# Optimization experiments

Hardware: AMD Instinct MI355X
Metric: run time of the kernel (lower is better)

## Reference

```python
import math
import jax, jax.numpy as jnp
import numpy as np

HIDDEN = 2048
NUM_HEADS = 16
HEAD_DIM = HIDDEN // NUM_HEADS  # 128
KV_RANK = 512
ROPE_DIM = 64
MAX_POS = 131072
ORIG_POS = 8192
BASE = 500000.0
BETA_FAST, BETA_SLOW = 32.0, 1.0
B, S = 2, 2048
EPS = 1e-6


def yarn_inv_freq():
    scaling = MAX_POS / ORIG_POS
    pos_freqs = BASE ** (np.arange(0, ROPE_DIM, 2, dtype=np.float64) / ROPE_DIM)
    extrap = 1.0 / pos_freqs
    interp = 1.0 / (scaling * pos_freqs)
    low = max(math.floor(ROPE_DIM * math.log(ORIG_POS / (BETA_FAST * 2 * math.pi)) / (2 * math.log(BASE))), 0)
    high = min(math.ceil(ROPE_DIM * math.log(ORIG_POS / (BETA_SLOW * 2 * math.pi)) / (2 * math.log(BASE))), ROPE_DIM - 1)
    i = np.arange(ROPE_DIM // 2, dtype=np.float64)
    smooth = np.clip((i - low) / max(high - low, 1), 0.0, 1.0)
    inv_freq = (1.0 - smooth) * interp + smooth * extrap
    return np.asarray(inv_freq, dtype=np.float32)


def yarn_cos_sin(seq_len, dtype):
    inv_freq = jnp.asarray(yarn_inv_freq())  # [rope/2]
    pos = jnp.arange(seq_len, dtype=jnp.float32)
    freqs = pos[:, None] * inv_freq[None, :]          # [S, rope/2]
    emb = jnp.concatenate([freqs, freqs], axis=-1)    # [S, rope]
    scaling = MAX_POS / ORIG_POS
    mscale = (0.1 * math.log(scaling) + 1.0) if scaling > 1 else 1.0
    cos = (jnp.cos(emb) * mscale).astype(dtype)[None]  # [1, S, rope]
    sin = (jnp.sin(emb) * mscale).astype(dtype)[None]
    return cos, sin


def rotate_half(x):
    x1, x2 = jnp.split(x, 2, axis=-1)
    return jnp.concatenate([-x2, x1], axis=-1)


def rms_norm(x, w):
    xf = x.astype(jnp.float32)
    var = jnp.mean(xf * xf, axis=-1, keepdims=True)
    return (w * (xf * jax.lax.rsqrt(var + EPS))).astype(x.dtype)


def setup_inputs() -> dict:
    key = jax.random.key(0)
    ks = jax.random.split(key, 5)
    return {
        'hidden_states': jax.random.normal(ks[0], (B, S, HIDDEN), jnp.float32),
        'q_w': jax.random.normal(ks[1], (NUM_HEADS * HEAD_DIM, HIDDEN), jnp.float32) * 0.02,
        'kv_a_w': jax.random.normal(ks[2], (KV_RANK + ROPE_DIM, HIDDEN), jnp.float32) * 0.02,
        'kv_b_w': jax.random.normal(ks[3], (NUM_HEADS * HEAD_DIM * 2, KV_RANK), jnp.float32) * 0.02,
        'o_w': jax.random.normal(ks[4], (HIDDEN, NUM_HEADS * HEAD_DIM), jnp.float32) * 0.02,
        'kv_norm_w': jnp.ones((KV_RANK,), jnp.float32),
    }


def reference(hidden_states, q_w, kv_a_w, kv_b_w, o_w, kv_norm_w):
    b, s, _ = hidden_states.shape
    # Q projection -> [B, H, S, D]
    q = hidden_states @ q_w.T
    q = q.reshape(b, s, NUM_HEADS, HEAD_DIM).transpose(0, 2, 1, 3)
    # KV compression: split off rope part (unused, matching source) and latent
    kv_compress = hidden_states @ kv_a_w.T               # [B, S, rope + rank]
    kv_latent = kv_compress[..., ROPE_DIM:]              # [B, S, rank]
    kv_latent = rms_norm(kv_latent, kv_norm_w)
    kv = kv_latent @ kv_b_w.T                            # [B, S, H*D*2]
    kv = kv.reshape(b, s, NUM_HEADS, 2, HEAD_DIM)
    k = kv[:, :, :, 0].transpose(0, 2, 1, 3)             # [B, H, S, D]
    v = kv[:, :, :, 1].transpose(0, 2, 1, 3)
    # Partial RoPE on first ROPE_DIM dims
    cos, sin = yarn_cos_sin(s, q.dtype)                  # [1, S, rope]
    cos = cos[:, None]                                   # [1, 1, S, rope]
    sin = sin[:, None]
    q_pe, k_pe = q[..., :ROPE_DIM], k[..., :ROPE_DIM]
    q_pe = q_pe * cos + rotate_half(q_pe) * sin
    k_pe = k_pe * cos + rotate_half(k_pe) * sin
    q = jnp.concatenate([q_pe, q[..., ROPE_DIM:]], axis=-1)
    k = jnp.concatenate([k_pe, k[..., ROPE_DIM:]], axis=-1)
    # SDPA (no mask), softmax in fp32
    scale = HEAD_DIM ** -0.5
    scores = jnp.einsum('bhqd,bhkd->bhqk', q, k) * scale
    attn = jax.nn.softmax(scores.astype(jnp.float32), axis=-1).astype(q.dtype)
    out = jnp.einsum('bhqk,bhkd->bhqd', attn, v)         # [B, H, S, D]
    out = out.transpose(0, 2, 1, 3).reshape(b, s, NUM_HEADS * HEAD_DIM)
    return out @ o_w.T
```

## Files before the change

### kernel.cpp

```cpp
#include <hip/hip_runtime.h>

typedef unsigned short u16;
typedef unsigned int u32;
typedef __attribute__((ext_vector_type(4))) float f32x4;
typedef __attribute__((ext_vector_type(8))) short short8;

#define S_LEN 2048
#define BATCH 2
#define HID 2048
#define NH 16
#define HD 128
#define KVR 512
#define TOKENS 4096
#define QSCALE 0.12751879523243842f

__device__ __forceinline__ u32 f2bf(float f) {
  u32 b = __float_as_uint(f);
  return (b + 0x7FFFu + ((b >> 16) & 1u)) >> 16;
}
__device__ __forceinline__ float bf2f(u16 u) {
  return __uint_as_float(((u32)u) << 16);
}
__device__ __forceinline__ void gl16(const void* g, void* l) {
  __builtin_amdgcn_global_load_lds((const __attribute__((address_space(1))) void*)g,
                                   (__attribute__((address_space(3))) void*)l, 16, 0, 0);
}
__device__ __forceinline__ u32 cvtpk(float a, float b) {
  u32 r;
  asm("v_cvt_pk_bf16_f32 %0, %1, %2" : "=v"(r) : "v"(a), "v"(b));
  return r;
}

__global__ __launch_bounds__(256) void convert_f32_bf16(const float* __restrict__ in,
                                                        u16* __restrict__ out, int n4) {
  int stride = gridDim.x * blockDim.x;
  for (int i = blockIdx.x * blockDim.x + threadIdx.x; i < n4; i += stride) {
    float4 v = reinterpret_cast<const float4*>(in)[i];
    uint2 o;
    o.x = f2bf(v.x) | (f2bf(v.y) << 16);
    o.y = f2bf(v.z) | (f2bf(v.w) << 16);
    reinterpret_cast<uint2*>(out)[i] = o;
  }
}

__global__ __launch_bounds__(256) void yarn_table(float2* __restrict__ cs) {
  int idx = blockIdx.x * blockDim.x + threadIdx.x;
  if (idx >= S_LEN * 32) return;
  int pos = idx >> 5, i = idx & 31;
  double pf = pow(500000.0, (double)i / 32.0);
  double sm = ((double)i - 9.0) / 9.0;
  sm = sm < 0.0 ? 0.0 : (sm > 1.0 ? 1.0 : sm);
  double invf = (1.0 - sm) / (16.0 * pf) + sm / pf;
  float f = (float)pos * (float)invf;
  const float mscale = 1.2772588722239781f;
  cs[idx] = make_float2(cosf(f) * mscale, sinf(f) * mscale);
}

__global__ __launch_bounds__(256) void rmsnorm_kernel(const float* __restrict__ X,
                                                      const float* __restrict__ w,
                                                      u16* __restrict__ out) {
  int wid = threadIdx.x >> 6, lane = threadIdx.x & 63;
  int row = blockIdx.x * 4 + wid;
  const float* xr = X + (size_t)row * KVR;
  float4 v0 = reinterpret_cast<const float4*>(xr)[lane * 2];
  float4 v1 = reinterpret_cast<const float4*>(xr)[lane * 2 + 1];
  float ss = v0.x * v0.x + v0.y * v0.y + v0.z * v0.z + v0.w * v0.w +
             v1.x * v1.x + v1.y * v1.y + v1.z * v1.z + v1.w * v1.w;
  #pragma unroll
  for (int m = 1; m < 64; m <<= 1) ss += __shfl_xor(ss, m);
  float sc = rsqrtf(ss * (1.0f / KVR) + 1e-6f);
  const float* wr = w + lane * 8;
  uint4 o;
  o.x = f2bf(v0.x * sc * wr[0]) | (f2bf(v0.y * sc * wr[1]) << 16);
  o.y = f2bf(v0.z * sc * wr[2]) | (f2bf(v0.w * sc * wr[3]) << 16);
  o.z = f2bf(v1.x * sc * wr[4]) | (f2bf(v1.y * sc * wr[5]) << 16);
  o.w = f2bf(v1.z * sc * wr[6]) | (f2bf(v1.w * sc * wr[7]) << 16);
  reinterpret_cast<uint4*>(out)[(size_t)row * 64 + lane] = o;
}

__global__ __launch_bounds__(256) void vtrans_kernel(const u16* __restrict__ kv,
                                                     u16* __restrict__ Vt) {
  __shared__ u16 T[128 * 128];
  const int bh = blockIdx.y, b = bh >> 4, h = bh & 15;
  const int s0 = blockIdx.x * 128;
  const int tid = threadIdx.x;
  const u16* src = kv + ((size_t)(b * S_LEN + s0)) * 4096 + h * 256 + 128;
  #pragma unroll
  for (int c = 0; c < 8; ++c) {
    int u = c * 256 + tid;
    int row = u >> 4, slot = u & 15;
    uint4 v = *reinterpret_cast<const uint4*>(src + (size_t)row * 4096 + slot * 8);
    *reinterpret_cast<uint4*>(&T[row * 128 + ((slot ^ (row & 7)) << 3)]) = v;
  }
  __syncthreads();
  #pragma unroll
  for (int c = 0; c < 8; ++c) {
    int u = c * 256 + tid;
    int d = u >> 4, j = u & 15;
    u16 tmp[8] __attribute__((aligned(16)));
    #pragma unroll
    for (int i = 0; i < 8; ++i) {
      int s = j * 8 + i;
      tmp[i] = T[s * 128 + (((d >> 3) ^ (s & 7)) << 3) + (d & 7)];
    }
    *reinterpret_cast<uint4*>(Vt + ((size_t)bh * 128 + d) * S_LEN + s0 + j * 8) =
        *reinterpret_cast<const uint4*>(tmp);
  }
}

template<int MODE>
__global__ __launch_bounds__(256) void gemm_bt(const u16* __restrict__ A,
                                               const u16* __restrict__ W,
                                               void* __restrict__ C0v,
                                               void* __restrict__ C1v,
                                               const float2* __restrict__ cs,
                                               int M, int N, int K) {
  __shared__ u16 As[128 * 32];
  __shared__ u16 Bs[128 * 32];
  const int tid = threadIdx.x;
  const int wid = tid >> 6;
  const int lane = tid & 63;
  const int r16 = lane & 15;
  const int kg = lane >> 4;
  const int bm = blockIdx.y * 128;
  const int bn = blockIdx.x * 128;
  const int wm = (wid >> 1) * 64;
  const int wn = (wid & 1) * 64;
  f32x4 acc[4][4] = {};
  const int srow = tid >> 2;
  const int sslot = tid & 3;
  const int ra = srow, rb = 64 + srow;
  const int ca = sslot ^ ((ra >> 1) & 3);
  const int cb = sslot ^ ((rb >> 1) & 3);
  const u16* a0 = A + (size_t)(bm + ra) * K + ca * 8;
  const u16* a1 = A + (size_t)(bm + rb) * K + cb * 8;
  const u16* b0 = W + (size_t)(bn + ra) * K + ca * 8;
  const u16* b1 = W + (size_t)(bn + rb) * K + cb * 8;

  for (int kt = 0; kt < K; kt += 32) {
    gl16(a0 + kt, &As[wid * 512]);
    gl16(a1 + kt, &As[wid * 512 + 2048]);
    gl16(b0 + kt, &Bs[wid * 512]);
    gl16(b1 + kt, &Bs[wid * 512 + 2048]);
    __syncthreads();
    short8 af[4], bfv[4];
    #pragma unroll
    for (int mi = 0; mi < 4; ++mi) {
      int row = wm + mi * 16 + r16;
      af[mi] = *reinterpret_cast<const short8*>(&As[row * 32 + ((kg ^ ((row >> 1) & 3)) << 3)]);
    }
    #pragma unroll
    for (int ni = 0; ni < 4; ++ni) {
      int row = wn + ni * 16 + r16;
      bfv[ni] = *reinterpret_cast<const short8*>(&Bs[row * 32 + ((kg ^ ((row >> 1) & 3)) << 3)]);
    }
    #pragma unroll
    for (int mi = 0; mi < 4; ++mi)
      #pragma unroll
      for (int ni = 0; ni < 4; ++ni)
        acc[mi][ni] = __builtin_amdgcn_mfma_f32_16x16x32_bf16(af[mi], bfv[ni], acc[mi][ni], 0, 0, 0);
    __syncthreads();
  }

  if (MODE == 2 || MODE == 3) {
    const bool doRope = (wn == 0) && (MODE == 2 ? (bn < 2048) : ((bn & 128) == 0));
    if (doRope) {
      #pragma unroll
      for (int mi = 0; mi < 4; ++mi) {
        const int t0 = bm + wm + mi * 16 + kg * 4;
        #pragma unroll
        for (int r = 0; r < 4; ++r) {
          const int pos = (t0 + r) & (S_LEN - 1);
          #pragma unroll
          for (int np = 0; np < 2; ++np) {
            float2 c = cs[pos * 32 + np * 16 + r16];
            float x1 = acc[mi][np][r], x2 = acc[mi][np + 2][r];
            acc[mi][np][r] = x1 * c.x - x2 * c.y;
            acc[mi][np + 2][r] = x2 * c.x + x1 * c.y;
          }
        }
      }
    }
  }

  if (MODE == 1) {
    float* C = (float*)C0v;
    #pragma unroll
    for (int mi = 0; mi < 4; ++mi)
      #pragma unroll
      for (int ni = 0; ni < 4; ++ni) {
        size_t base = (size_t)(bm + wm + mi * 16 + kg * 4) * N + (bn + wn + ni * 16 + r16);
        #pragma unroll
        for (int r = 0; r < 4; ++r) C[base + (size_t)r * N] = acc[mi][ni][r];
      }
  } else if (MODE == 2) {
    if (bn < 2048) {
      u16* C = (u16*)C0v;
      #pragma unroll
      for (int mi = 0; mi < 4; ++mi)
        #pragma unroll
        for (int ni = 0; ni < 4; ++ni) {
          size_t base = (size_t)(bm + wm + mi * 16 + kg * 4) * HID + (bn + wn + ni * 16 + r16);
          #pragma unroll
          for (int r = 0; r < 4; ++r) C[base + (size_t)r * HID] = (u16)f2bf(acc[mi][ni][r] * QSCALE);
        }
    } else {
      float* C = (float*)C1v;
      #pragma unroll
      for (int mi = 0; mi < 4; ++mi)
        #pragma unroll
        for (int ni = 0; ni < 4; ++ni) {
          size_t base = (size_t)(bm + wm + mi * 16 + kg * 4) * KVR +
                        (bn - 2048 + wn + ni * 16 + r16);
          #pragma unroll
          for (int r = 0; r < 4; ++r) C[base + (size_t)r * KVR] = acc[mi][ni][r];
        }
    }
  } else {
    u16* C = (u16*)C0v;
    #pragma unroll
    for (int mi = 0; mi < 4; ++mi)
      #pragma unroll
      for (int ni = 0; ni < 4; ++ni) {
        size_t base = (size_t)(bm + wm + mi * 16 + kg * 4) * N + (bn + wn + ni * 16 + r16);
        #pragma unroll
        for (int r = 0; r < 4; ++r) C[base + (size_t)r * N] = (u16)f2bf(acc[mi][ni][r]);
      }
  }
}

#define KVB 64
__global__ __launch_bounds__(256) void attn_kernel(const u16* __restrict__ Q,
                                                   const u16* __restrict__ KV,
                                                   const u16* __restrict__ Vt,
                                                   u16* __restrict__ O) {
  __shared__ u16 Ks[2][KVB * 128];
  __shared__ u16 Vs[2][128 * KVB];
  __shared__ u16 Ps[4][2][16 * 64];
  const int tid = threadIdx.x, wid = tid >> 6, lane = tid & 63;
  const int r16 = lane & 15, kg = lane >> 4;
  const int bh = blockIdx.x, b = bh >> 4, h = bh & 15;
  const int q0 = blockIdx.y * 128 + wid * 32;

  short8 qf0[4], qf1[4];
  {
    const size_t qr0 = ((size_t)(b * S_LEN) + q0 + r16) * HID + h * HD;
    #pragma unroll
    for (int ds = 0; ds < 4; ++ds) {
      qf0[ds] = *reinterpret_cast<const short8*>(&Q[qr0 + ds * 32 + kg * 8]);
      qf1[ds] = *reinterpret_cast<const short8*>(&Q[qr0 + (size_t)16 * HID + ds * 32 + kg * 8]);
    }
  }
  asm volatile("s_waitcnt vmcnt(0)" ::: "memory");

  f32x4 oacc0[8] = {}, oacc1[8] = {};
  float m0 = -3.0e38f, l0 = 0.0f, m1 = -3.0e38f, l1 = 0.0f;

  const int krow = wid * 4 + (lane >> 4);
  const int kslot = (lane & 15) ^ (krow & 7);
  const u16* gK = KV + (size_t)(b * S_LEN) * 4096 + h * 256 + (size_t)krow * 4096 + kslot * 8;
  const int vrow = wid * 8 + (lane >> 3);
  const int vslot = (lane & 7) ^ (vrow & 7);
  const u16* gV = Vt + ((size_t)bh * 128 + vrow) * S_LEN + vslot * 8;

  auto stage = [&](int buf, int it) {
    const int k0 = it * KVB;
    #pragma unroll
    for (int c = 0; c < 4; ++c) {
      gl16(gK + (size_t)(k0 + c * 16) * 4096, &Ks[buf][(c * 256 + wid * 64) * 8]);
      gl16(gV + (size_t)c * 32 * S_LEN + k0, &Vs[buf][(c * 256 + wid * 64) * 8]);
    }
  };

  auto qk = [&](const u16* Kc, short8 (&qf)[4], f32x4 (&sc)[4]) {
    #pragma unroll
    for (int nt = 0; nt < 4; ++nt) {
      sc[nt] = (f32x4){0.f, 0.f, 0.f, 0.f};
      const int key = nt * 16 + r16;
      #pragma unroll
      for (int ds = 0; ds < 4; ++ds) {
        short8 kf = *reinterpret_cast<const short8*>(
            &Kc[key * 128 + (((ds * 4 + kg) ^ (r16 & 7)) << 3)]);
        sc[nt] = __builtin_amdgcn_mfma_f32_16x16x32_bf16(kf, qf[ds], sc[nt], 0, 0, 0);
      }
    }
  };

  auto softmax_store = [&](f32x4 (&sc)[4], float& mreg, float& lreg, f32x4 (&oa)[8],
                           u16* psbase) {
    float mx = fmaxf(fmaxf(fmaxf(sc[0][0], sc[0][1]), fmaxf(sc[0][2], sc[0][3])),
                     fmaxf(fmaxf(sc[1][0], sc[1][1]), fmaxf(sc[1][2], sc[1][3])));
    mx = fmaxf(mx, fmaxf(fmaxf(fmaxf(sc[2][0], sc[2][1]), fmaxf(sc[2][2], sc[2][3])),
                         fmaxf(fmaxf(sc[3][0], sc[3][1]), fmaxf(sc[3][2], sc[3][3]))));
    mx = fmaxf(mx, __shfl_xor(mx, 16));
    mx = fmaxf(mx, __shfl_xor(mx, 32));
    if (!__all(mx - mreg <= 8.0f)) {
      float nm = fmaxf(mreg, mx);
      float al = __builtin_amdgcn_exp2f(mreg - nm);
      mreg = nm;
      lreg *= al;
      float ar0 = __shfl(al, kg * 4 + 0), ar1 = __shfl(al, kg * 4 + 1);
      float ar2 = __shfl(al, kg * 4 + 2), ar3 = __shfl(al, kg * 4 + 3);
      #pragma unroll
      for (int db = 0; db < 8; ++db) {
        oa[db][0] *= ar0; oa[db][1] *= ar1; oa[db][2] *= ar2; oa[db][3] *= ar3;
      }
    }
    const float nm = mreg;
    float s0 = 0.f;
    #pragma unroll
    for (int nt = 0; nt < 4; ++nt) {
      float p0 = __builtin_amdgcn_exp2f(sc[nt][0] - nm);
      float p1 = __builtin_amdgcn_exp2f(sc[nt][1] - nm);
      float p2 = __builtin_amdgcn_exp2f(sc[nt][2] - nm);
      float p3 = __builtin_amdgcn_exp2f(sc[nt][3] - nm);
      s0 += (p0 + p1) + (p2 + p3);
      uint2 pk;
      pk.x = cvtpk(p0, p1);
      pk.y = cvtpk(p2, p3);
      *reinterpret_cast<uint2*>(
          &psbase[(r16 * 64 + nt * 16 + kg * 4) ^ ((r16 & 7) << 3)]) = pk;
    }
    s0 += __shfl_xor(s0, 16);
    s0 += __shfl_xor(s0, 32);
    lreg += s0;
  };

  stage(0, 0);
  for (int it = 0; it < S_LEN / KVB; ++it) {
    const int cur = it & 1;
    if (it + 1 < S_LEN / KVB) {
      stage(cur ^ 1, it + 1);
      asm volatile("s_waitcnt vmcnt(8)" ::: "memory");
    } else {
      asm volatile("s_waitcnt vmcnt(0)" ::: "memory");
    }
    __builtin_amdgcn_s_barrier();

    const u16* Kc = &Ks[cur][0];
    f32x4 sc[4];
    qk(Kc, qf0, sc);
    softmax_store(sc, m0, l0, oacc0, &Ps[wid][0][0]);
    __builtin_amdgcn_sched_barrier(0);
    qk(Kc, qf1, sc);
    softmax_store(sc, m1, l1, oacc1, &Ps[wid][1][0]);
    __builtin_amdgcn_sched_barrier(0);

    const u16* Vc = &Vs[cur][0];
    #pragma unroll
    for (int ks = 0; ks < 2; ++ks) {
      const int pidx = (r16 * 64 + ks * 32 + kg * 8) ^ ((r16 & 7) << 3);
      short8 pa0 = *reinterpret_cast<const short8*>(&Ps[wid][0][pidx]);
      short8 pa1 = *reinterpret_cast<const short8*>(&Ps[wid][1][pidx]);
      #pragma unroll
      for (int db = 0; db < 8; ++db) {
        const int drow = db * 16 + r16;
        short8 vf = *reinterpret_cast<const short8*>(
            &Vc[drow * 64 + (((ks * 4 + kg) ^ (r16 & 7)) << 3)]);
        oacc0[db] = __builtin_amdgcn_mfma_f32_16x16x32_bf16(pa0, vf, oacc0[db], 0, 0, 0);
        oacc1[db] = __builtin_amdgcn_mfma_f32_16x16x32_bf16(pa1, vf, oacc1[db], 0, 0, 0);
      }
    }
    __builtin_amdgcn_s_barrier();
  }

  {
    float li0 = 1.0f / l0, li1 = 1.0f / l1;
    float lr0[4], lr1[4];
    #pragma unroll
    for (int r = 0; r < 4; ++r) {
      lr0[r] = __shfl(li0, kg * 4 + r);
      lr1[r] = __shfl(li1, kg * 4 + r);
    }
    #pragma unroll
    for (int db = 0; db < 8; ++db)
      #pragma unroll
      for (int r = 0; r < 4; ++r) {
        size_t i0 = ((size_t)(b * S_LEN) + q0 + kg * 4 + r) * HID + h * HD + db * 16 + r16;
        O[i0] = (u16)f2bf(oacc0[db][r] * lr0[r]);
        O[i0 + (size_t)16 * HID] = (u16)f2bf(oacc1[db][r] * lr1[r]);
      }
  }
}

extern "C" void kernel_launch(void* const* d_in, const int* in_sizes, int n_in,
                              void* d_out, int out_size, void* d_ws, size_t ws_size,
                              hipStream_t stream) {
  (void)in_sizes; (void)n_in; (void)out_size; (void)ws_size;
  const float* hidden = (const float*)d_in[0];
  const float* q_w    = (const float*)d_in[1];
  const float* kv_a_w = (const float*)d_in[2];
  const float* kv_b_w = (const float*)d_in[3];
  const float* o_w    = (const float*)d_in[4];
  const float* nw     = (const float*)d_in[5];

  char* ws = (char*)d_ws;
  size_t off = 0;
  auto carve = [&](size_t n) { void* p = ws + off; off += (n + 255) & ~(size_t)255; return p; };
  u16* h_bf    = (u16*)carve((size_t)TOKENS * HID * 2);
  u16* qaw_bf  = (u16*)carve((size_t)2560 * HID * 2);
  u16* kvbw_bf = (u16*)carve((size_t)4096 * KVR * 2);
  u16* ow_bf   = (u16*)carve((size_t)HID * HID * 2);
  u16* q_bf    = (u16*)carve((size_t)TOKENS * HID * 2);
  float* lat_f = (float*)carve((size_t)TOKENS * KVR * 4);
  u16* lat_bf  = (u16*)carve((size_t)TOKENS * KVR * 2);
  u16* kv_bf   = (u16*)carve((size_t)TOKENS * 4096 * 2);
  float2* cs_t = (float2*)carve((size_t)S_LEN * 32 * 8);
  u16* attn_bf = (u16*)carve((size_t)TOKENS * HID * 2);
  u16* vt_bf   = h_bf;

  dim3 blk(256);
  auto cg = [](int n4) { int g = (n4 + 255) / 256; return dim3(g > 2048 ? 2048 : g); };

  convert_f32_bf16<<<cg(TOKENS * HID / 4), blk, 0, stream>>>(hidden, h_bf, TOKENS * HID / 4);
  convert_f32_bf16<<<cg(HID * HID / 4), blk, 0, stream>>>(q_w, qaw_bf, HID * HID / 4);
  convert_f32_bf16<<<cg(KVR * HID / 4), blk, 0, stream>>>(kv_a_w + 64 * HID,
                                                          qaw_bf + (size_t)2048 * HID,
                                                          KVR * HID / 4);
  convert_f32_bf16<<<cg(4096 * KVR / 4), blk, 0, stream>>>(kv_b_w, kvbw_bf, 4096 * KVR / 4);
  convert_f32_bf16<<<cg(HID * HID / 4), blk, 0, stream>>>(o_w, ow_bf, HID * HID / 4);
  yarn_table<<<dim3(S_LEN * 32 / 256), blk, 0, stream>>>(cs_t);

  gemm_bt<2><<<dim3(2560 / 128, TOKENS / 128), blk, 0, stream>>>(
      h_bf, qaw_bf, q_bf, lat_f, cs_t, TOKENS, 2560, HID);
  rmsnorm_kernel<<<dim3(TOKENS / 4), blk, 0, stream>>>(lat_f, nw, lat_bf);
  gemm_bt<3><<<dim3(4096 / 128, TOKENS / 128), blk, 0, stream>>>(
      lat_bf, kvbw_bf, kv_bf, nullptr, cs_t, TOKENS, 4096, KVR);

  vtrans_kernel<<<dim3(S_LEN / 128, BATCH * NH), blk, 0, stream>>>(kv_bf, vt_bf);

  attn_kernel<<<dim3(BATCH * NH, S_LEN / 128), blk, 0, stream>>>(q_bf, kv_bf, vt_bf, attn_bf);

  gemm_bt<1><<<dim3(HID / 128, TOKENS / 128), blk, 0, stream>>>(
      attn_bf, ow_bf, (float*)d_out, nullptr, cs_t, TOKENS, HID, HID);
}
```

Baseline: 304.9 us.

## Use 32x32 MFMA in attention and fuse V transpose into kv GEMM epilogue

```diff
diff --git a/kernel.cpp b/kernel.cpp
--- a/kernel.cpp
+++ b/kernel.cpp
@@ -3,6 +3,7 @@
 typedef unsigned short u16;
 typedef unsigned int u32;
 typedef __attribute__((ext_vector_type(4))) float f32x4;
+typedef __attribute__((ext_vector_type(16))) float f32x16;
 typedef __attribute__((ext_vector_type(8))) short short8;
 
 #define S_LEN 2048
@@ -76,36 +77,6 @@
   o.z = f2bf(v1.x * sc * wr[4]) | (f2bf(v1.y * sc * wr[5]) << 16);
   o.w = f2bf(v1.z * sc * wr[6]) | (f2bf(v1.w * sc * wr[7]) << 16);
   reinterpret_cast<uint4*>(out)[(size_t)row * 64 + lane] = o;
-}
-
-__global__ __launch_bounds__(256) void vtrans_kernel(const u16* __restrict__ kv,
-                                                     u16* __restrict__ Vt) {
-  __shared__ u16 T[128 * 128];
-  const int bh = blockIdx.y, b = bh >> 4, h = bh & 15;
-  const int s0 = blockIdx.x * 128;
-  const int tid = threadIdx.x;
-  const u16* src = kv + ((size_t)(b * S_LEN + s0)) * 4096 + h * 256 + 128;
-  #pragma unroll
-  for (int c = 0; c < 8; ++c) {
-    int u = c * 256 + tid;
-    int row = u >> 4, slot = u & 15;
-    uint4 v = *reinterpret_cast<const uint4*>(src + (size_t)row * 4096 + slot * 8);
-    *reinterpret_cast<uint4*>(&T[row * 128 + ((slot ^ (row & 7)) << 3)]) = v;
-  }
-  __syncthreads();
-  #pragma unroll
-  for (int c = 0; c < 8; ++c) {
-    int u = c * 256 + tid;
-    int d = u >> 4, j = u & 15;
-    u16 tmp[8] __attribute__((aligned(16)));
-    #pragma unroll
-    for (int i = 0; i < 8; ++i) {
-      int s = j * 8 + i;
-      tmp[i] = T[s * 128 + (((d >> 3) ^ (s & 7)) << 3) + (d & 7)];
-    }
-    *reinterpret_cast<uint4*>(Vt + ((size_t)bh * 128 + d) * S_LEN + s0 + j * 8) =
-        *reinterpret_cast<const uint4*>(tmp);
-  }
 }
 
 template<int MODE>
@@ -216,6 +187,35 @@
           for (int r = 0; r < 4; ++r) C[base + (size_t)r * KVR] = acc[mi][ni][r];
         }
     }
+  } else if (MODE == 3) {
+    if ((bn & 128) == 0) {
+      u16* C = (u16*)C0v;
+      #pragma unroll
+      for (int mi = 0; mi < 4; ++mi)
+        #pragma unroll
+        for (int ni = 0; ni < 4; ++ni) {
+          size_t base = (size_t)(bm + wm + mi * 16 + kg * 4) * N + (bn + wn + ni * 16 + r16);
+          #pragma unroll
+          for (int r = 0; r < 4; ++r) C[base + (size_t)r * N] = (u16)f2bf(acc[mi][ni][r]);
+        }
+    } else {
+      u16* Vt = (u16*)C1v;
+      const int hh = bn >> 8;
+      #pragma unroll
+      for (int mi = 0; mi < 4; ++mi) {
+        const int tok0 = bm + wm + mi * 16 + kg * 4;
+        const int bb = tok0 >> 11, s = tok0 & (S_LEN - 1);
+        #pragma unroll
+        for (int ni = 0; ni < 4; ++ni) {
+          const int d = wn + ni * 16 + r16;
+          uint2 pk;
+          pk.x = cvtpk(acc[mi][ni][0], acc[mi][ni][1]);
+          pk.y = cvtpk(acc[mi][ni][2], acc[mi][ni][3]);
+          *reinterpret_cast<uint2*>(
+              &Vt[((size_t)((bb * 16 + hh) * 128 + d)) * S_LEN + s]) = pk;
+        }
+      }
+    }
   } else {
     u16* C = (u16*)C0v;
     #pragma unroll
@@ -236,25 +236,23 @@
                                                    u16* __restrict__ O) {
   __shared__ u16 Ks[2][KVB * 128];
   __shared__ u16 Vs[2][128 * KVB];
-  __shared__ u16 Ps[4][2][16 * 64];
+  __shared__ u16 Ps[4][32 * 64];
   const int tid = threadIdx.x, wid = tid >> 6, lane = tid & 63;
-  const int r16 = lane & 15, kg = lane >> 4;
+  const int q = lane & 31, hi = lane >> 5;
   const int bh = blockIdx.x, b = bh >> 4, h = bh & 15;
   const int q0 = blockIdx.y * 128 + wid * 32;
 
-  short8 qf0[4], qf1[4];
+  short8 qf[8];
   {
-    const size_t qr0 = ((size_t)(b * S_LEN) + q0 + r16) * HID + h * HD;
-    #pragma unroll
-    for (int ds = 0; ds < 4; ++ds) {
-      qf0[ds] = *reinterpret_cast<const short8*>(&Q[qr0 + ds * 32 + kg * 8]);
-      qf1[ds] = *reinterpret_cast<const short8*>(&Q[qr0 + (size_t)16 * HID + ds * 32 + kg * 8]);
-    }
+    const size_t qr = ((size_t)(b * S_LEN) + q0 + q) * HID + h * HD;
+    #pragma unroll
+    for (int ds = 0; ds < 8; ++ds)
+      qf[ds] = *reinterpret_cast<const short8*>(&Q[qr + ds * 16 + hi * 8]);
   }
   asm volatile("s_waitcnt vmcnt(0)" ::: "memory");
 
-  f32x4 oacc0[8] = {}, oacc1[8] = {};
-  float m0 = -3.0e38f, l0 = 0.0f, m1 = -3.0e38f, l1 = 0.0f;
+  f32x16 oacc[4] = {};
+  float m = -3.0e38f, l = 0.0f;
 
   const int krow = wid * 4 + (lane >> 4);
   const int kslot = (lane & 15) ^ (krow & 7);
@@ -270,60 +268,6 @@
       gl16(gK + (size_t)(k0 + c * 16) * 4096, &Ks[buf][(c * 256 + wid * 64) * 8]);
       gl16(gV + (size_t)c * 32 * S_LEN + k0, &Vs[buf][(c * 256 + wid * 64) * 8]);
     }
-  };
-
-  auto qk = [&](const u16* Kc, short8 (&qf)[4], f32x4 (&sc)[4]) {
-    #pragma unroll
-    for (int nt = 0; nt < 4; ++nt) {
-      sc[nt] = (f32x4){0.f, 0.f, 0.f, 0.f};
-      const int key = nt * 16 + r16;
-      #pragma unroll
-      for (int ds = 0; ds < 4; ++ds) {
-        short8 kf = *reinterpret_cast<const short8*>(
-            &Kc[key * 128 + (((ds * 4 + kg) ^ (r16 & 7)) << 3)]);
-        sc[nt] = __builtin_amdgcn_mfma_f32_16x16x32_bf16(kf, qf[ds], sc[nt], 0, 0, 0);
-      }
-    }
-  };
-
-  auto softmax_store = [&](f32x4 (&sc)[4], float& mreg, float& lreg, f32x4 (&oa)[8],
-                           u16* psbase) {
-    float mx = fmaxf(fmaxf(fmaxf(sc[0][0], sc[0][1]), fmaxf(sc[0][2], sc[0][3])),
-                     fmaxf(fmaxf(sc[1][0], sc[1][1]), fmaxf(sc[1][2], sc[1][3])));
-    mx = fmaxf(mx, fmaxf(fmaxf(fmaxf(sc[2][0], sc[2][1]), fmaxf(sc[2][2], sc[2][3])),
-                         fmaxf(fmaxf(sc[3][0], sc[3][1]), fmaxf(sc[3][2], sc[3][3]))));
-    mx = fmaxf(mx, __shfl_xor(mx, 16));
-    mx = fmaxf(mx, __shfl_xor(mx, 32));
-    if (!__all(mx - mreg <= 8.0f)) {
-      float nm = fmaxf(mreg, mx);
-      float al = __builtin_amdgcn_exp2f(mreg - nm);
-      mreg = nm;
-      lreg *= al;
-      float ar0 = __shfl(al, kg * 4 + 0), ar1 = __shfl(al, kg * 4 + 1);
-      float ar2 = __shfl(al, kg * 4 + 2), ar3 = __shfl(al, kg * 4 + 3);
-      #pragma unroll
-      for (int db = 0; db < 8; ++db) {
-        oa[db][0] *= ar0; oa[db][1] *= ar1; oa[db][2] *= ar2; oa[db][3] *= ar3;
-      }
-    }
-    const float nm = mreg;
-    float s0 = 0.f;
-    #pragma unroll
-    for (int nt = 0; nt < 4; ++nt) {
-      float p0 = __builtin_amdgcn_exp2f(sc[nt][0] - nm);
-      float p1 = __builtin_amdgcn_exp2f(sc[nt][1] - nm);
-      float p2 = __builtin_amdgcn_exp2f(sc[nt][2] - nm);
-      float p3 = __builtin_amdgcn_exp2f(sc[nt][3] - nm);
-      s0 += (p0 + p1) + (p2 + p3);
-      uint2 pk;
-      pk.x = cvtpk(p0, p1);
-      pk.y = cvtpk(p2, p3);
-      *reinterpret_cast<uint2*>(
-          &psbase[(r16 * 64 + nt * 16 + kg * 4) ^ ((r16 & 7) << 3)]) = pk;
-    }
-    s0 += __shfl_xor(s0, 16);
-    s0 += __shfl_xor(s0, 32);
-    lreg += s0;
   };
 
   stage(0, 0);
@@ -338,48 +282,90 @@
     __builtin_amdgcn_s_barrier();
 
     const u16* Kc = &Ks[cur][0];
-    f32x4 sc[4];
-    qk(Kc, qf0, sc);
-    softmax_store(sc, m0, l0, oacc0, &Ps[wid][0][0]);
-    __builtin_amdgcn_sched_barrier(0);
-    qk(Kc, qf1, sc);
-    softmax_store(sc, m1, l1, oacc1, &Ps[wid][1][0]);
-    __builtin_amdgcn_sched_barrier(0);
-
     const u16* Vc = &Vs[cur][0];
-    #pragma unroll
-    for (int ks = 0; ks < 2; ++ks) {
-      const int pidx = (r16 * 64 + ks * 32 + kg * 8) ^ ((r16 & 7) << 3);
-      short8 pa0 = *reinterpret_cast<const short8*>(&Ps[wid][0][pidx]);
-      short8 pa1 = *reinterpret_cast<const short8*>(&Ps[wid][1][pidx]);
-      #pragma unroll
-      for (int db = 0; db < 8; ++db) {
-        const int drow = db * 16 + r16;
+    u16* Pw = &Ps[wid][0];
+
+    #pragma unroll
+    for (int kt = 0; kt < 2; ++kt) {
+      f32x16 st = {};
+      #pragma unroll
+      for (int ds = 0; ds < 8; ++ds) {
+        short8 kf = *reinterpret_cast<const short8*>(
+            &Kc[(kt * 32 + q) * 128 + (((ds * 2 + hi) ^ (q & 7)) << 3)]);
+        st = __builtin_amdgcn_mfma_f32_32x32x16_bf16(kf, qf[ds], st, 0, 0, 0);
+      }
+      float mx = fmaxf(fmaxf(fmaxf(st[0], st[1]), fmaxf(st[2], st[3])),
+                       fmaxf(fmaxf(st[4], st[5]), fmaxf(st[6], st[7])));
+      mx = fmaxf(mx, fmaxf(fmaxf(fmaxf(st[8], st[9]), fmaxf(st[10], st[11])),
+                           fmaxf(fmaxf(st[12], st[13]), fmaxf(st[14], st[15]))));
+      mx = fmaxf(mx, __shfl_xor(mx, 32));
+      if (!__all(mx - m <= 8.0f)) {
+        float nm = fmaxf(m, mx);
+        float al = __builtin_amdgcn_exp2f(m - nm);
+        m = nm;
+        l *= al;
+        #pragma unroll
+        for (int dt = 0; dt < 4; ++dt)
+          #pragma unroll
+          for (int g = 0; g < 16; ++g) oacc[dt][g] *= al;
+      }
+      float s0 = 0.f;
+      #pragma unroll
+      for (int g4 = 0; g4 < 4; ++g4) {
+        float p0 = __builtin_amdgcn_exp2f(st[g4 * 4 + 0] - m);
+        float p1 = __builtin_amdgcn_exp2f(st[g4 * 4 + 1] - m);
+        float p2 = __builtin_amdgcn_exp2f(st[g4 * 4 + 2] - m);
+        float p3 = __builtin_amdgcn_exp2f(st[g4 * 4 + 3] - m);
+        s0 += (p0 + p1) + (p2 + p3);
+        uint2 pk;
+        pk.x = cvtpk(p0, p1);
+        pk.y = cvtpk(p2, p3);
+        *reinterpret_cast<uint2*>(
+            &Pw[q * 64 + ((kt * 32 + g4 * 8 + hi * 4) ^ (8 * (q & 7)))]) = pk;
+      }
+      s0 += __shfl_xor(s0, 32);
+      l += s0;
+      __builtin_amdgcn_sched_barrier(0);
+    }
+
+    #pragma unroll
+    for (int kt16 = 0; kt16 < 4; ++kt16) {
+      short8 pf = *reinterpret_cast<const short8*>(
+          &Pw[q * 64 + ((kt16 * 16 + hi * 8) ^ (8 * (q & 7)))]);
+      #pragma unroll
+      for (int dt = 0; dt < 4; ++dt) {
         short8 vf = *reinterpret_cast<const short8*>(
-            &Vc[drow * 64 + (((ks * 4 + kg) ^ (r16 & 7)) << 3)]);
-        oacc0[db] = __builtin_amdgcn_mfma_f32_16x16x32_bf16(pa0, vf, oacc0[db], 0, 0, 0);
-        oacc1[db] = __builtin_amdgcn_mfma_f32_16x16x32_bf16(pa1, vf, oacc1[db], 0, 0, 0);
+            &Vc[(dt * 32 + q) * 64 + (((kt16 * 2 + hi) ^ (q & 7)) << 3)]);
+        oacc[dt] = __builtin_amdgcn_mfma_f32_32x32x16_bf16(vf, pf, oacc[dt], 0, 0, 0);
       }
     }
     __builtin_amdgcn_s_barrier();
   }
 
   {
-    float li0 = 1.0f / l0, li1 = 1.0f / l1;
-    float lr0[4], lr1[4];
-    #pragma unroll
-    for (int r = 0; r < 4; ++r) {
-      lr0[r] = __shfl(li0, kg * 4 + r);
-      lr1[r] = __shfl(li1, kg * 4 + r);
-    }
-    #pragma unroll
-    for (int db = 0; db < 8; ++db)
-      #pragma unroll
-      for (int r = 0; r < 4; ++r) {
-        size_t i0 = ((size_t)(b * S_LEN) + q0 + kg * 4 + r) * HID + h * HD + db * 16 + r16;
-        O[i0] = (u16)f2bf(oacc0[db][r] * lr0[r]);
-        O[i0 + (size_t)16 * HID] = (u16)f2bf(oacc1[db][r] * lr1[r]);
-      }
+    const float linv = 1.0f / l;
+    u16* T = &Ps[wid][0];
+    const size_t orow = ((size_t)(b * S_LEN) + q0 + q) * HID + h * HD;
+    #pragma unroll
+    for (int p = 0; p < 2; ++p) {
+      #pragma unroll
+      for (int dth = 0; dth < 2; ++dth) {
+        const int dt = p * 2 + dth;
+        #pragma unroll
+        for (int g2 = 0; g2 < 8; ++g2) {
+          const int g = g2 * 2;
+          const int dl = dth * 32 + (g & 3) + 8 * (g >> 2) + 4 * hi;
+          u32 pk = cvtpk(oacc[dt][g] * linv, oacc[dt][g + 1] * linv);
+          *reinterpret_cast<u32*>(&T[q * 64 + (dl ^ (8 * (q & 7)))]) = pk;
+        }
+      }
+      #pragma unroll
+      for (int c = 0; c < 4; ++c) {
+        const int dl = hi * 8 + c * 16;
+        uint4 v = *reinterpret_cast<const uint4*>(&T[q * 64 + (dl ^ (8 * (q & 7)))]);
+        *reinterpret_cast<uint4*>(&O[orow + p * 64 + dl]) = v;
+      }
+    }
   }
 }
 
@@ -425,9 +411,7 @@
       h_bf, qaw_bf, q_bf, lat_f, cs_t, TOKENS, 2560, HID);
   rmsnorm_kernel<<<dim3(TOKENS / 4), blk, 0, stream>>>(lat_f, nw, lat_bf);
   gemm_bt<3><<<dim3(4096 / 128, TOKENS / 128), blk, 0, stream>>>(
-      lat_bf, kvbw_bf, kv_bf, nullptr, cs_t, TOKENS, 4096, KVR);
-
-  vtrans_kernel<<<dim3(S_LEN / 128, BATCH * NH), blk, 0, stream>>>(kv_bf, vt_bf);
+      lat_bf, kvbw_bf, kv_bf, vt_bf, cs_t, TOKENS, 4096, KVR);
 
   attn_kernel<<<dim3(BATCH * NH, S_LEN / 128), blk, 0, stream>>>(q_bf, kv_bf, vt_bf, attn_bf);
 
```

After: 319.7 us. 4.8% more time.
